# Performance work log

Hardware: AMD Instinct MI355X
Metric: run time of the kernel (lower is better)

## Reference

```python
import jax, jax.numpy as jnp
from jax import lax
import numpy as np

NINF = -1e10  # matches torch's -10000000000.0 masked fill


def setup_inputs() -> dict:
    B, T, Z, S1, X = 512, 1024, 8, 5, 2  # S1 = 2**stim_types + 1
    key = jax.random.key(0)
    k1, k2, k3, k4, k5, k6 = jax.random.split(key, 6)
    s = jax.random.randint(k1, (B, T), 0, S1)
    x = jax.random.randint(k2, (B, T), 0, X)
    mask = (jax.random.uniform(k3, (B, T)) > 0.1).astype(jnp.float32)
    # probability-simplex parameters (the torch model stores normalized pi/P/K)
    pi = jax.nn.softmax(jax.random.normal(k4, (Z,)))
    P = jax.nn.softmax(jax.random.normal(k5, (Z, X)), axis=-1)
    K = jax.nn.softmax(jax.random.normal(k6, (S1, Z, Z)), axis=-2)  # columns sum to 1 over 'to'
    return {"s": s, "x": x, "mask": mask, "pi": pi, "P": P, "K": K}


def reference(s, x, mask, pi, P, K):
    B, T = x.shape
    Z = pi.shape[0]
    logpi = jnp.log(pi)
    logP = jnp.log(P)            # (Z, X)
    logKb = jnp.log(K)[s]        # (B, T, Z, Z), [to, from]
    logPx = logP.T[x]            # (B, T, Z)

    # ---- forward pass: masked alpha recurrence ----
    def fstep(prev, inp):
        lK, lP, m = inp          # (B,Z,Z), (B,Z), (B,)
        new = (jax.nn.logsumexp(prev[:, None, :] + lK, axis=-1) + lP) * m[:, None] \
              + prev * (1.0 - m)[:, None]
        return new, new

    prev0 = jnp.broadcast_to(logpi[None, :], (B, Z))
    _, alphas = lax.scan(fstep, prev0,
                         (logKb.transpose(1, 0, 2, 3), logPx.transpose(1, 0, 2), mask.T))
    log_alpha = alphas.transpose(1, 0, 2)                 # (B, T, Z)
    loglik = jax.nn.logsumexp(log_alpha[:, -1, :], axis=-1)  # (B,)

    # ---- backward pass: masked beta recurrence (carries masked P/K 'next') ----
    def bstep(carry, inp):
        bn, lPn, lKn = carry
        lK_t, lP_t, m0, m1 = inp  # mask[t], mask[t+1]
        bt = jax.nn.logsumexp(lPn[:, :, None] + lKn + bn[:, :, None], axis=1) * m1[:, None] \
             + bn * (1.0 - m1)[:, None]
        lPn2 = lP_t * m0[:, None] + lPn * (1.0 - m0)[:, None]
        lKn2 = lK_t * m0[:, None, None] + lKn * (1.0 - m0)[:, None, None]
        return (bt, lPn2, lKn2), bt

    carry0 = (jnp.zeros((B, Z)), logPx[:, -1], logKb[:, -1])
    xs = (logKb[:, :-1].transpose(1, 0, 2, 3), logPx[:, :-1].transpose(1, 0, 2),
          mask[:, :-1].T, mask[:, 1:].T)
    _, betas = lax.scan(bstep, carry0, xs, reverse=True)
    log_beta = jnp.concatenate([betas.transpose(1, 0, 2), jnp.zeros((B, 1, Z))], axis=1)

    # ---- posteriors ----
    log_beta = log_beta - loglik[:, None, None]
    log_gamma = log_alpha + log_beta
    log_gamma = log_gamma - jax.nn.logsumexp(log_gamma, axis=-1, keepdims=True)
    log_xi = logKb[:, :-1] + log_alpha[:, :-1, :, None] + log_beta[:, 1:, None, :] \
             + logPx[:, 1:][:, :, None, :]
    log_xi = log_xi - jax.nn.logsumexp(log_xi.reshape(B, T - 1, -1), axis=-1)[:, :, None, None]
    log_gamma = jnp.where((mask == 0)[:, :, None], NINF, log_gamma)
    log_xi = jnp.where((mask[:, 1:] == 0)[:, :, None, None], NINF, log_xi)
    return log_gamma, log_xi, log_alpha, log_beta, loglik
```

## Files before the change

### kernel.cpp

```cpp
#include <hip/hip_runtime.h>

#define BB 512
#define TT 1024
#define GG 32
#define LL 32
#define NINF -10000000000.0f

typedef float fvec4 __attribute__((ext_vector_type(4)));

template<int CTRL>
__device__ __forceinline__ float dppf(float x) {
    return __builtin_bit_cast(float, __builtin_amdgcn_update_dpp(
        0, __builtin_bit_cast(int, x), CTRL, 0xF, 0xF, true));
}
__device__ __forceinline__ float gsum8(float x) {
    x += dppf<0xB1>(x); x += dppf<0x4E>(x); x += dppf<0x141>(x); return x;
}
__device__ __forceinline__ float gmax8(float x) {
    x = fmaxf(x, dppf<0xB1>(x)); x = fmaxf(x, dppf<0x4E>(x)); x = fmaxf(x, dppf<0x141>(x)); return x;
}

#define GATHER8(A0, A1, A2, A3, A4, A5, A6, A7)      \
    const float A1 = dppf<0xB1>(A0);                 \
    const float A2 = dppf<0x4E>(A0);                 \
    const float A7 = dppf<0x141>(A0);                \
    const float A3 = dppf<0x4E>(A1);                 \
    const float A6 = dppf<0xB1>(A7);                 \
    const float A5 = dppf<0x4E>(A7);                 \
    const float A4 = dppf<0x4E>(A6);

#define FMASUM(ACC, K0, K1, A0,A1,A2,A3,A4,A5,A6,A7) \
    float ACC;                                       \
    {   float accA = K0.x * A0;                      \
        accA = fmaf(K0.y, A1, accA);                 \
        accA = fmaf(K0.z, A2, accA);                 \
        accA = fmaf(K0.w, A3, accA);                 \
        float accB = K1.x * A4;                      \
        accB = fmaf(K1.y, A5, accB);                 \
        accB = fmaf(K1.z, A6, accB);                 \
        ACC = accA + accB; }

__global__ __launch_bounds__(256) void segmat_kernel(
    const int* __restrict__ s, const int* __restrict__ x, const float* __restrict__ mask,
    const float* __restrict__ P, const float* __restrict__ K,
    float* __restrict__ FM, float* __restrict__ BM)
{
    __shared__ float kTab[5 * 68];
    __shared__ int   ctrlA[4][LL];
    const int tid = threadIdx.x;
    const int wv = tid >> 6, l = tid & 63;
    const int lo = l & 7, hi = l >> 3;
    const bool isF = blockIdx.x < 4096;
    const int task = (isF ? blockIdx.x : blockIdx.x - 4096) * 4 + wv;
    const int seq = task >> 5, seg = task & 31;
    const int sb = seq * TT;
    const int t0 = seg * LL;

    for (int e = tid; e < 340; e += 256) {
        const int ss = e / 68, idx = e - ss * 68;
        float v = 0.0f;
        if (idx < 64) {
            const int row = idx >> 3, r = idx & 7;
            v = isF ? K[ss*64 + row*8 + (row ^ r)]
                    : K[ss*64 + (row ^ r)*8 + row];
        }
        kTab[e] = v;
    }
    if (l < LL) {
        const int tt = t0 + l;
        ctrlA[wv][l] = s[sb+tt] | (x[sb+tt] << 3) | ((mask[sb+tt] != 0.0f) ? 16 : 0);
    }
    __syncthreads();

    const float pL0 = P[lo*2+0], pL1 = P[lo*2+1];
    const float* kbase = kTab + lo*8;
    float av = (lo == hi) ? 1.0f : 0.0f;
    float c = 0.0f;

    if (isF) {
#pragma unroll 4
        for (int u = 0; u < LL; ++u) {
            const int cw = __builtin_amdgcn_readfirstlane(ctrlA[wv][u]);
            if (cw & 16) {
                const float* kp = kbase + (cw & 7) * 68;
                const float4 k0 = *(const float4*)kp;
                const float4 k1 = *(const float4*)(kp + 4);
                const float a0 = av;
                GATHER8(a0, a1, a2, a3, a4, a5, a6, a7)
                FMASUM(acc, k0, k1, a0,a1,a2,a3,a4,a5,a6,a7)
                av = acc * ((cw & 8) ? pL1 : pL0);
            }
            if ((u & 3) == 3) {
                const float ms = gmax8(av);
                av *= __builtin_amdgcn_rcpf(ms);
                c += __logf(ms);
            }
        }
        FM[task*64 + l] = __logf(av) + c;
    } else {
        const int t1 = t0 + LL;
        int sxc = 0;
        for (int tt = t1; tt < TT; ++tt) {
            if (mask[sb + tt] != 0.0f) { sxc = s[sb+tt] | (x[sb+tt] << 3); break; }
        }
        int m1 = (t1 < TT && mask[sb + t1] != 0.0f) ? 16 : 0;
        sxc = __builtin_amdgcn_readfirstlane(sxc);
        m1  = __builtin_amdgcn_readfirstlane(m1);
#pragma unroll 4
        for (int u = LL - 1; u >= 0; --u) {
            const int cw = __builtin_amdgcn_readfirstlane(ctrlA[wv][u]);
            if (m1) {
                const float* kp = kbase + (sxc & 7) * 68;
                const float4 k0 = *(const float4*)kp;
                const float4 k1 = *(const float4*)(kp + 4);
                const float u0 = av * ((sxc & 8) ? pL1 : pL0);
                GATHER8(u0, u1, u2, u3, u4, u5, u6, u7)
                FMASUM(acc, k0, k1, u0,u1,u2,u3,u4,u5,u6,u7)
                av = acc;
            }
            sxc = (cw & 16) ? (cw & 15) : sxc;
            m1 = cw & 16;
            if ((u & 3) == 0) {
                const float ms = gmax8(av);
                av *= __builtin_amdgcn_rcpf(ms);
                c += __logf(ms);
            }
        }
        BM[task*64 + l] = __logf(av) + c;
    }
}

__global__ __launch_bounds__(256) void compose_kernel(
    const float* __restrict__ pi, const float* __restrict__ FM, const float* __restrict__ BM,
    float* __restrict__ SV, float* __restrict__ WV, float* __restrict__ loglik)
{
    const int tid = threadIdx.x;
    const int grp = blockIdx.x * 32 + (tid >> 3);
    const int i = tid & 7;
    if (grp < BB) {
        const int seq = grp;
        float v = __logf(pi[i]);
        for (int g = 0; g < GG; ++g) {
            SV[(seq*GG + g)*8 + i] = v;
            const float* M = FM + (size_t)(seq*GG + g) * 64;
            const float a0 = v;
            GATHER8(a0, a1, a2, a3, a4, a5, a6, a7)
            const float q0 = M[(i^0)*8 + i] + a0;
            const float q1 = M[(i^1)*8 + i] + a1;
            const float q2 = M[(i^2)*8 + i] + a2;
            const float q3 = M[(i^3)*8 + i] + a3;
            const float q4 = M[(i^4)*8 + i] + a4;
            const float q5 = M[(i^5)*8 + i] + a5;
            const float q6 = M[(i^6)*8 + i] + a6;
            const float q7 = M[(i^7)*8 + i] + a7;
            float m = fmaxf(q0, q1); m = fmaxf(m, q2); m = fmaxf(m, q3);
            m = fmaxf(m, q4); m = fmaxf(m, q5); m = fmaxf(m, q6); m = fmaxf(m, q7);
            float sum = __expf(q0-m) + __expf(q1-m) + __expf(q2-m) + __expf(q3-m)
                      + __expf(q4-m) + __expf(q5-m) + __expf(q6-m) + __expf(q7-m);
            v = m + __logf(sum);
        }
        const float gm = gmax8(v);
        const float ge = gsum8(__expf(v - gm));
        if (i == 0) loglik[seq] = gm + __logf(ge);
    } else {
        const int seq = grp - BB;
        float v = 0.0f;
        for (int g = GG - 1; g >= 0; --g) {
            WV[(seq*GG + g)*8 + i] = v;
            const float* M = BM + (size_t)(seq*GG + g) * 64;
            const float a0 = v;
            GATHER8(a0, a1, a2, a3, a4, a5, a6, a7)
            const float q0 = M[(i^0)*8 + i] + a0;
            const float q1 = M[(i^1)*8 + i] + a1;
            const float q2 = M[(i^2)*8 + i] + a2;
            const float q3 = M[(i^3)*8 + i] + a3;
            const float q4 = M[(i^4)*8 + i] + a4;
            const float q5 = M[(i^5)*8 + i] + a5;
            const float q6 = M[(i^6)*8 + i] + a6;
            const float q7 = M[(i^7)*8 + i] + a7;
            float m = fmaxf(q0, q1); m = fmaxf(m, q2); m = fmaxf(m, q3);
            m = fmaxf(m, q4); m = fmaxf(m, q5); m = fmaxf(m, q6); m = fmaxf(m, q7);
            float sum = __expf(q0-m) + __expf(q1-m) + __expf(q2-m) + __expf(q3-m)
                      + __expf(q4-m) + __expf(q5-m) + __expf(q6-m) + __expf(q7-m);
            v = m + __logf(sum);
        }
    }
}

__global__ __launch_bounds__(256) void replay_kernel(
    const int* __restrict__ s, const int* __restrict__ x, const float* __restrict__ mask,
    const float* __restrict__ P, const float* __restrict__ K,
    const float* __restrict__ SV, const float* __restrict__ WV,
    const float* __restrict__ loglik,
    float* __restrict__ alpha, float* __restrict__ beta)
{
    __shared__ float kTab[5 * 68];
    __shared__ int   ctrlC[4][LL * 8];
    const int tid = threadIdx.x;
    const int wv = tid >> 6, l = tid & 63;
    const int lo = l & 7, g = l >> 3;
    const bool isF = blockIdx.x < 512;
    const int task = (isF ? blockIdx.x : blockIdx.x - 512) * 4 + wv;
    const int sgp = task >> 5, seg = task & 31;
    const int bfirst = sgp * 8;
    const int seq = bfirst + g;
    const int sb = seq * TT;
    const int t0 = seg * LL;

    for (int e = tid; e < 340; e += 256) {
        const int ss = e / 68, idx = e - ss * 68;
        float v = 0.0f;
        if (idx < 64) {
            const int row = idx >> 3, r = idx & 7;
            v = isF ? K[ss*64 + row*8 + (row ^ r)]
                    : K[ss*64 + (row ^ r)*8 + row];
        }
        kTab[e] = v;
    }
    for (int e = l; e < LL * 8; e += 64) {
        const int slot = e >> 3, gg = e & 7;
        const int adr = (bfirst + gg) * TT + t0 + slot;
        ctrlC[wv][e] = s[adr] | (x[adr] << 3) | ((mask[adr] != 0.0f) ? 16 : 0);
    }
    __syncthreads();

    const float pL0 = P[lo*2+0], pL1 = P[lo*2+1];
    const float* kbase = kTab + lo*8;

    if (isF) {
        const float sv0 = SV[(seq*GG + seg)*8 + lo];
        const float mx = gmax8(sv0);
        float av = __expf(sv0 - mx);
        float c = mx;
        int aoff = (sb + t0) * 8 + lo;
#pragma unroll 4
        for (int u = 0; u < LL; ++u) {
            const int cw = ctrlC[wv][u*8 + g];
            const float* kp = kbase + (cw & 7) * 68;
            const float4 k0 = *(const float4*)kp;
            const float4 k1 = *(const float4*)(kp + 4);
            const float a0 = av;
            GATHER8(a0, a1, a2, a3, a4, a5, a6, a7)
            FMASUM(acc, k0, k1, a0,a1,a2,a3,a4,a5,a6,a7)
            const float nv = acc * ((cw & 8) ? pL1 : pL0);
            av = (cw & 16) ? nv : av;
            if ((u & 3) == 3) {
                const float ms = gmax8(av);
                av *= __builtin_amdgcn_rcpf(ms);
                c += __logf(ms);
            }
            alpha[aoff] = __logf(av) + c;
            aoff += 8;
        }
    } else {
        const float wv0 = WV[(seq*GG + seg)*8 + lo];
        const float ll = loglik[seq];
        const float mx = gmax8(wv0);
        float bv = __expf(wv0 - mx);
        float c = mx - ll;
        const int t1 = t0 + LL;
        int m1 = 0, sxc = 0;
        if (t1 < TT) m1 = (mask[sb + t1] != 0.0f) ? 16 : 0;
        {
            int tt = t1;
            int found = (t1 >= TT) ? 1 : 0;
            while (!__all(found)) {
                if (!found && tt < TT) {
                    if (mask[sb + tt] != 0.0f) { sxc = s[sb+tt] | (x[sb+tt] << 3); found = 1; }
                }
                if (tt >= TT - 1) found = 1;
                ++tt;
            }
        }
        int boff = (sb + t1 - 1) * 8 + lo;
#pragma unroll 4
        for (int u = LL - 1; u >= 0; --u) {
            const int cw = ctrlC[wv][u*8 + g];
            const float* kp = kbase + (sxc & 7) * 68;
            const float4 k0 = *(const float4*)kp;
            const float4 k1 = *(const float4*)(kp + 4);
            const float u0 = bv * ((sxc & 8) ? pL1 : pL0);
            GATHER8(u0, u1, u2, u3, u4, u5, u6, u7)
            FMASUM(acc, k0, k1, u0,u1,u2,u3,u4,u5,u6,u7)
            bv = m1 ? acc : bv;
            if ((u & 3) == 0) {
                const float ms = gmax8(bv);
                bv *= __builtin_amdgcn_rcpf(ms);
                c += __logf(ms);
            }
            beta[boff] = __logf(bv) + c;
            boff -= 8;
            sxc = (cw & 16) ? (cw & 15) : sxc;
            m1 = cw & 16;
        }
    }
}

__global__ __launch_bounds__(256) void post_kernel(
    const int* __restrict__ s, const int* __restrict__ x, const float* __restrict__ mask,
    const float* __restrict__ P, const float* __restrict__ K,
    const float* __restrict__ alpha, const float* __restrict__ beta,
    float* __restrict__ gamma, float* __restrict__ xi)
{
    __shared__ float lK[320];
    __shared__ float lP0[8], lP1[8];
    const int tid = threadIdx.x;
    for (int e = tid; e < 320; e += 256) lK[e] = __logf(K[e]);
    if (tid < 8) { lP0[tid] = __logf(P[tid*2]); lP1[tid] = __logf(P[tid*2+1]); }
    __syncthreads();

    const int w = blockIdx.x * 4 + (tid >> 6);
    const int l = tid & 63;
    const int b = w >> 8;
    const int t0 = (w & 255) * 4;
    const long bt0 = (long)b * TT + t0;

    if (l < 32) {
        const int qg = l >> 3, z = l & 7;
        const long bt = bt0 + qg;
        const float m0 = mask[bt];
        const float a = alpha[bt*8 + z];
        const float bb = beta[bt*8 + z];
        __builtin_nontemporal_store((m0 != 0.0f) ? (a + bb) : NINF, &gamma[bt*8 + z]);
    }
    const int q = l >> 4, ll = l & 15;
    const long t = t0 + q;
    const long bt = bt0 + q;
    const bool wx = (t < TT - 1);
    const long tn = wx ? (bt + 1) : bt;
    const float m1 = mask[tn];
    const int svv = s[bt];
    const int xv = x[tn];
    const int i = ll >> 1;
    const int bj = (ll & 1) * 4;
    float4 out;
    if (wx && m1 != 0.0f) {
        const float aHi = alpha[bt*8 + i];
        const float4 bN = *(const float4*)&beta[tn*8 + bj];
        const float4 kv = *(const float4*)&lK[svv*64 + ll*4];
        const float4 p0 = *(const float4*)&lP0[bj];
        const float4 p1 = *(const float4*)&lP1[bj];
        out.x = kv.x + aHi + bN.x + (xv ? p1.x : p0.x);
        out.y = kv.y + aHi + bN.y + (xv ? p1.y : p0.y);
        out.z = kv.z + aHi + bN.z + (xv ? p1.z : p0.z);
        out.w = kv.w + aHi + bN.w + (xv ? p1.w : p0.w);
    } else {
        out.x = NINF; out.y = NINF; out.z = NINF; out.w = NINF;
    }
    if (wx) __builtin_nontemporal_store(__builtin_bit_cast(fvec4, out),
                (fvec4*)&xi[((long)b*(TT-1) + t)*64 + ll*4]);
}

extern "C" void kernel_launch(void* const* d_in, const int* in_sizes, int n_in,
                              void* d_out, int out_size, void* d_ws, size_t ws_size,
                              hipStream_t stream) {
    const int*   s    = (const int*)d_in[0];
    const int*   x    = (const int*)d_in[1];
    const float* mask = (const float*)d_in[2];
    const float* pi   = (const float*)d_in[3];
    const float* P    = (const float*)d_in[4];
    const float* K    = (const float*)d_in[5];

    float* out    = (float*)d_out;
    float* gamma  = out;
    float* xi     = gamma + (size_t)BB * TT * 8;
    float* alpha  = xi + (size_t)BB * (TT - 1) * 64;
    float* beta   = alpha + (size_t)BB * TT * 8;
    float* loglik = beta + (size_t)BB * TT * 8;

    float* FMs = xi + (size_t)31000000;
    float* BMs = FMs + (size_t)BB * GG * 64;
    float* SVs = BMs + (size_t)BB * GG * 64;
    float* WVs = SVs + (size_t)BB * GG * 8;

    segmat_kernel<<<8192, 256, 0, stream>>>(s, x, mask, P, K, FMs, BMs);
    compose_kernel<<<32, 256, 0, stream>>>(pi, FMs, BMs, SVs, WVs, loglik);
    replay_kernel<<<1024, 256, 0, stream>>>(s, x, mask, P, K, SVs, WVs, loglik, alpha, beta);
    post_kernel<<<BB * TT / 16, 256, 0, stream>>>(s, x, mask, P, K, alpha, beta, gamma, xi);
}
```

Baseline: 128.8 us.

## Fuse posterior gamma/xi computation into alpha/beta replay kernel via shared memory

Merges the replay and post kernels. Each block now runs paired forward and backward segments for the same 32-step window, stages alpha and beta in LDS, and then writes gamma and xi straight from shared memory. This avoids re-reading alpha and beta from global memory and removes one kernel launch. Scratch space moves to the workspace when it is large enough; otherwise a small fixup kernel recomputes the xi rows that overlap the scratch area. The trade-off is much higher LDS use per block, which may lower occupancy, and the xi store loop is serialized per wave.

```diff
diff --git a/kernel.cpp b/kernel.cpp
--- a/kernel.cpp
+++ b/kernel.cpp
@@ -5,8 +5,9 @@
 #define GG 32
 #define LL 32
 #define NINF -10000000000.0f
-
-typedef float fvec4 __attribute__((ext_vector_type(4)));
+#define SROW 65
+#define NXROWS (BB * (TT - 1))
+#define SCRATCH_ROW0 484375
 
 template<int CTRL>
 __device__ __forceinline__ float dppf(float x) {
@@ -187,56 +188,70 @@
     }
 }
 
-__global__ __launch_bounds__(256) void replay_kernel(
+__global__ __launch_bounds__(256) void fused_kernel(
     const int* __restrict__ s, const int* __restrict__ x, const float* __restrict__ mask,
     const float* __restrict__ P, const float* __restrict__ K,
     const float* __restrict__ SV, const float* __restrict__ WV,
     const float* __restrict__ loglik,
-    float* __restrict__ alpha, float* __restrict__ beta)
+    float* __restrict__ alpha, float* __restrict__ beta,
+    float* __restrict__ gamma, float* __restrict__ xi, int skipRow0)
 {
-    __shared__ float kTab[5 * 68];
-    __shared__ int   ctrlC[4][LL * 8];
+    __shared__ float aLs[2 * 32 * SROW];
+    __shared__ float bLs[2 * 33 * SROW];
+    __shared__ int   ctrlL[2 * 33 * 8];
+    __shared__ float kX[340], kTt[340];
+    __shared__ float lK[320], lP[16];
+
     const int tid = threadIdx.x;
     const int wv = tid >> 6, l = tid & 63;
     const int lo = l & 7, g = l >> 3;
-    const bool isF = blockIdx.x < 512;
-    const int task = (isF ? blockIdx.x : blockIdx.x - 512) * 4 + wv;
-    const int sgp = task >> 5, seg = task & 31;
+    const int sgp = blockIdx.x >> 4;
+    const int pairIdx = blockIdx.x & 15;
     const int bfirst = sgp * 8;
+    const int segi = wv >> 1;
+    const bool isFwd = (wv & 1) == 0;
+    const int seg = pairIdx * 2 + segi;
+    const int t0 = seg * LL;
     const int seq = bfirst + g;
     const int sb = seq * TT;
-    const int t0 = seg * LL;
 
     for (int e = tid; e < 340; e += 256) {
         const int ss = e / 68, idx = e - ss * 68;
-        float v = 0.0f;
+        float vX = 0.0f, vT = 0.0f;
         if (idx < 64) {
             const int row = idx >> 3, r = idx & 7;
-            v = isF ? K[ss*64 + row*8 + (row ^ r)]
-                    : K[ss*64 + (row ^ r)*8 + row];
-        }
-        kTab[e] = v;
-    }
-    for (int e = l; e < LL * 8; e += 64) {
-        const int slot = e >> 3, gg = e & 7;
-        const int adr = (bfirst + gg) * TT + t0 + slot;
-        ctrlC[wv][e] = s[adr] | (x[adr] << 3) | ((mask[adr] != 0.0f) ? 16 : 0);
+            vX = K[ss*64 + row*8 + (row ^ r)];
+            vT = K[ss*64 + (row ^ r)*8 + row];
+        }
+        kX[e] = vX; kTt[e] = vT;
+    }
+    for (int e = tid; e < 320; e += 256) lK[e] = __logf(K[e]);
+    if (tid < 16) lP[tid] = __logf(P[tid]);
+    for (int e = tid; e < 528; e += 256) {
+        const int si = e / 264, rem = e - si * 264;
+        const int u = rem >> 3, gg = rem & 7;
+        const int t = (pairIdx*2 + si)*LL + u;
+        int cv = 0;
+        if (t < TT) {
+            const int a = (bfirst + gg)*TT + t;
+            cv = s[a] | (x[a] << 3) | ((mask[a] != 0.0f) ? 16 : 0);
+        }
+        ctrlL[(si*33 + u)*8 + gg] = cv;
     }
     __syncthreads();
 
     const float pL0 = P[lo*2+0], pL1 = P[lo*2+1];
-    const float* kbase = kTab + lo*8;
-
-    if (isF) {
+
+    if (isFwd) {
         const float sv0 = SV[(seq*GG + seg)*8 + lo];
         const float mx = gmax8(sv0);
         float av = __expf(sv0 - mx);
         float c = mx;
-        int aoff = (sb + t0) * 8 + lo;
+        size_t aoff = (size_t)(sb + t0)*8 + lo;
 #pragma unroll 4
         for (int u = 0; u < LL; ++u) {
-            const int cw = ctrlC[wv][u*8 + g];
-            const float* kp = kbase + (cw & 7) * 68;
+            const int cw = ctrlL[(segi*33 + u)*8 + g];
+            const float* kp = kX + (cw & 7)*68 + lo*8;
             const float4 k0 = *(const float4*)kp;
             const float4 k1 = *(const float4*)(kp + 4);
             const float a0 = av;
@@ -249,18 +264,21 @@
                 av *= __builtin_amdgcn_rcpf(ms);
                 c += __logf(ms);
             }
-            alpha[aoff] = __logf(av) + c;
+            const float la = __logf(av) + c;
+            aLs[(segi*32 + u)*SROW + g*8 + lo] = la;
+            __builtin_nontemporal_store(la, &alpha[aoff]);
             aoff += 8;
         }
     } else {
-        const float wv0 = WV[(seq*GG + seg)*8 + lo];
-        const float ll = loglik[seq];
-        const float mx = gmax8(wv0);
-        float bv = __expf(wv0 - mx);
-        float c = mx - ll;
+        const float w0 = WV[(seq*GG + seg)*8 + lo];
+        const float llv = loglik[seq];
+        const float mx = gmax8(w0);
+        float bv = __expf(w0 - mx);
+        float c = mx - llv;
+        bLs[(segi*33 + 32)*SROW + g*8 + lo] = w0 - llv;
         const int t1 = t0 + LL;
-        int m1 = 0, sxc = 0;
-        if (t1 < TT) m1 = (mask[sb + t1] != 0.0f) ? 16 : 0;
+        int m1 = ctrlL[(segi*33 + 32)*8 + g] & 16;
+        int sxc = 0;
         {
             int tt = t1;
             int found = (t1 >= TT) ? 1 : 0;
@@ -272,11 +290,11 @@
                 ++tt;
             }
         }
-        int boff = (sb + t1 - 1) * 8 + lo;
+        size_t boff = (size_t)(sb + t1 - 1)*8 + lo;
 #pragma unroll 4
         for (int u = LL - 1; u >= 0; --u) {
-            const int cw = ctrlC[wv][u*8 + g];
-            const float* kp = kbase + (sxc & 7) * 68;
+            const int cw = ctrlL[(segi*33 + u)*8 + g];
+            const float* kp = kTt + (sxc & 7)*68 + lo*8;
             const float4 k0 = *(const float4*)kp;
             const float4 k1 = *(const float4*)(kp + 4);
             const float u0 = bv * ((sxc & 8) ? pL1 : pL0);
@@ -288,67 +306,73 @@
                 bv *= __builtin_amdgcn_rcpf(ms);
                 c += __logf(ms);
             }
-            beta[boff] = __logf(bv) + c;
+            const float lb = __logf(bv) + c;
+            bLs[(segi*33 + u)*SROW + g*8 + lo] = lb;
+            __builtin_nontemporal_store(lb, &beta[boff]);
             boff -= 8;
             sxc = (cw & 16) ? (cw & 15) : sxc;
             m1 = cw & 16;
         }
     }
-}
-
-__global__ __launch_bounds__(256) void post_kernel(
+    __syncthreads();
+
+    for (int it = 0; it < 16; ++it) {
+        const int r = wv*128 + it*8 + (l >> 3);
+        const int si = r >> 8, rr = r & 255, sq = rr >> 5, u = rr & 31;
+        const int t = (pairIdx*2 + si)*LL + u;
+        const int z = l & 7;
+        const int cw = ctrlL[(si*33 + u)*8 + sq];
+        const float gv = (cw & 16)
+            ? (aLs[(si*32 + u)*SROW + sq*8 + z] + bLs[(si*33 + u)*SROW + sq*8 + z])
+            : NINF;
+        __builtin_nontemporal_store(gv, &gamma[((size_t)(bfirst+sq)*TT + t)*8 + z]);
+    }
+    for (int it = 0; it < 128; ++it) {
+        const int r = wv*128 + it;
+        const int si = r >> 8, rr = r & 255, sq = rr >> 5, u = rr & 31;
+        const int t = (pairIdx*2 + si)*LL + u;
+        if (t >= TT - 1) continue;
+        const int rowLin = (bfirst + sq)*(TT - 1) + t;
+        if (rowLin >= skipRow0) continue;
+        const int cw  = ctrlL[(si*33 + u)*8 + sq];
+        const int cw1 = ctrlL[(si*33 + u + 1)*8 + sq];
+        float xo = NINF;
+        if (cw1 & 16) {
+            const float aHi = aLs[(si*32 + u)*SROW + sq*8 + (l >> 3)];
+            const float bN  = bLs[(si*33 + u + 1)*SROW + sq*8 + (l & 7)];
+            xo = lK[(cw & 7)*64 + l] + aHi + bN + lP[(l & 7)*2 + ((cw1 >> 3) & 1)];
+        }
+        __builtin_nontemporal_store(xo, &xi[(size_t)rowLin*64 + l]);
+    }
+}
+
+__global__ __launch_bounds__(256) void xi_fixup_kernel(
     const int* __restrict__ s, const int* __restrict__ x, const float* __restrict__ mask,
     const float* __restrict__ P, const float* __restrict__ K,
     const float* __restrict__ alpha, const float* __restrict__ beta,
-    float* __restrict__ gamma, float* __restrict__ xi)
+    float* __restrict__ xi)
 {
-    __shared__ float lK[320];
-    __shared__ float lP0[8], lP1[8];
+    __shared__ float lK[320], lP[16];
     const int tid = threadIdx.x;
     for (int e = tid; e < 320; e += 256) lK[e] = __logf(K[e]);
-    if (tid < 8) { lP0[tid] = __logf(P[tid*2]); lP1[tid] = __logf(P[tid*2+1]); }
+    if (tid < 16) lP[tid] = __logf(P[tid]);
     __syncthreads();
 
-    const int w = blockIdx.x * 4 + (tid >> 6);
-    const int l = tid & 63;
-    const int b = w >> 8;
-    const int t0 = (w & 255) * 4;
-    const long bt0 = (long)b * TT + t0;
-
-    if (l < 32) {
-        const int qg = l >> 3, z = l & 7;
-        const long bt = bt0 + qg;
-        const float m0 = mask[bt];
-        const float a = alpha[bt*8 + z];
-        const float bb = beta[bt*8 + z];
-        __builtin_nontemporal_store((m0 != 0.0f) ? (a + bb) : NINF, &gamma[bt*8 + z]);
-    }
-    const int q = l >> 4, ll = l & 15;
-    const long t = t0 + q;
-    const long bt = bt0 + q;
-    const bool wx = (t < TT - 1);
-    const long tn = wx ? (bt + 1) : bt;
-    const float m1 = mask[tn];
-    const int svv = s[bt];
-    const int xv = x[tn];
-    const int i = ll >> 1;
-    const int bj = (ll & 1) * 4;
-    float4 out;
-    if (wx && m1 != 0.0f) {
-        const float aHi = alpha[bt*8 + i];
-        const float4 bN = *(const float4*)&beta[tn*8 + bj];
-        const float4 kv = *(const float4*)&lK[svv*64 + ll*4];
-        const float4 p0 = *(const float4*)&lP0[bj];
-        const float4 p1 = *(const float4*)&lP1[bj];
-        out.x = kv.x + aHi + bN.x + (xv ? p1.x : p0.x);
-        out.y = kv.y + aHi + bN.y + (xv ? p1.y : p0.y);
-        out.z = kv.z + aHi + bN.z + (xv ? p1.z : p0.z);
-        out.w = kv.w + aHi + bN.w + (xv ? p1.w : p0.w);
-    } else {
-        out.x = NINF; out.y = NINF; out.z = NINF; out.w = NINF;
-    }
-    if (wx) __builtin_nontemporal_store(__builtin_bit_cast(fvec4, out),
-                (fvec4*)&xi[((long)b*(TT-1) + t)*64 + ll*4]);
+    const int wv = tid >> 6, l = tid & 63;
+    const int row = SCRATCH_ROW0 + blockIdx.x * 4 + wv;
+    if (row >= NXROWS) return;
+    const int b = row / (TT - 1);
+    const int t = row - b * (TT - 1);
+    const long bt = (long)b * TT + t;
+    float xo = NINF;
+    if (mask[bt + 1] != 0.0f) {
+        const int sv = s[bt];
+        const int xv = x[bt + 1];
+        const float aHi = alpha[bt*8 + (l >> 3)];
+        const float bN  = beta[(bt + 1)*8 + (l & 7)];
+        xo = lK[sv*64 + l] + aHi + bN + lP[(l & 7)*2 + xv];
+    }
+    xi[(size_t)row*64 + l] = xo;
 }
 
 extern "C" void kernel_launch(void* const* d_in, const int* in_sizes, int n_in,
@@ -368,13 +392,21 @@
     float* beta   = alpha + (size_t)BB * TT * 8;
     float* loglik = beta + (size_t)BB * TT * 8;
 
-    float* FMs = xi + (size_t)31000000;
+    const size_t scratchFloats = (size_t)2*BB*GG*64 + (size_t)2*BB*GG*8;
+    const bool useWs = ws_size >= scratchFloats * sizeof(float);
+    float* FMs = useWs ? (float*)d_ws : xi + (size_t)31000000;
     float* BMs = FMs + (size_t)BB * GG * 64;
     float* SVs = BMs + (size_t)BB * GG * 64;
     float* WVs = SVs + (size_t)BB * GG * 8;
+    const int skipRow0 = useWs ? 0x7FFFFFFF : SCRATCH_ROW0;
 
     segmat_kernel<<<8192, 256, 0, stream>>>(s, x, mask, P, K, FMs, BMs);
     compose_kernel<<<32, 256, 0, stream>>>(pi, FMs, BMs, SVs, WVs, loglik);
-    replay_kernel<<<1024, 256, 0, stream>>>(s, x, mask, P, K, SVs, WVs, loglik, alpha, beta);
-    post_kernel<<<BB * TT / 16, 256, 0, stream>>>(s, x, mask, P, K, alpha, beta, gamma, xi);
-}
+    fused_kernel<<<1024, 256, 0, stream>>>(s, x, mask, P, K, SVs, WVs, loglik,
+                                           alpha, beta, gamma, xi, skipRow0);
+    if (!useWs) {
+        const int tailRows = NXROWS - SCRATCH_ROW0;
+        xi_fixup_kernel<<<(tailRows + 3) / 4, 256, 0, stream>>>(
+            s, x, mask, P, K, alpha, beta, xi);
+    }
+}
```

Result: faster. 125.2 us (-2.8%).
